# Kernel optimization log

Measured on AMD Instinct MI355X. Metric: run time of the kernel, lower is better.

Reference implementation:

```python
import jax, jax.numpy as jnp
import numpy as np

B, S, D, H = 4, 2048, 1024, 16
DK = D // H


def setup_inputs() -> dict:
    key = jax.random.key(0)
    ks = jax.random.split(key, 12)
    std = 0.02
    inp = {
        "query": jax.random.normal(ks[0], (B, S, D), jnp.float32),
        "key": jax.random.normal(ks[1], (B, S, D), jnp.float32),
        "value": jax.random.normal(ks[2], (B, S, D), jnp.float32),
        "mask": jnp.ones((B, 1, 1, S), jnp.int32),
        "Wq": jax.random.normal(ks[3], (D, D), jnp.float32) * std,
        "bq": jnp.zeros((D,), jnp.float32),
        "Wk": jax.random.normal(ks[4], (D, D), jnp.float32) * std,
        "bk": jnp.zeros((D,), jnp.float32),
        "Wv": jax.random.normal(ks[5], (D, D), jnp.float32) * std,
        "bv": jnp.zeros((D,), jnp.float32),
        "Wo": jax.random.normal(ks[6], (D, D), jnp.float32) * std,
        "bo": jnp.zeros((D,), jnp.float32),
    }
    return inp


def reference(query, key, value, mask, Wq, bq, Wk, bk, Wv, bv, Wo, bo):
    # nn.Linear: x @ W.T + b; then split heads -> [B, H, S, DK]
    def proj(x, W, b):
        y = x @ W.T + b
        return y.reshape(B, S, H, DK).transpose(0, 2, 1, 3)

    q = proj(query, Wq, bq)
    k = proj(key, Wk, bk)
    v = proj(value, Wv, bv)

    scale = 1.0 / jnp.sqrt(jnp.asarray(DK, q.dtype))
    scores = jnp.einsum('bhqd,bhkd->bhqk', q, k) * scale  # [B,H,S,S]
    scores = jnp.where(mask == 0, jnp.asarray(-1e9, scores.dtype), scores)
    p_attn = jax.nn.softmax(scores, axis=-1)  # dropout p=0 -> identity
    ctx = jnp.einsum('bhqk,bhkd->bhqd', p_attn, v)
    ctx = ctx.transpose(0, 2, 1, 3).reshape(B, S, D)
    out = ctx @ Wo.T + bo
    return out
```

## Files before the change

kernel.cpp:

```cpp
#include <hip/hip_runtime.h>

#define BB 4
#define SS 2048
#define DD 1024
#define HH 16
#define DKC 64
#define MT (BB*SS)

typedef _Float16 f16x8 __attribute__((ext_vector_type(8)));
typedef _Float16 f16x4 __attribute__((ext_vector_type(4)));
typedef float f32x4 __attribute__((ext_vector_type(4)));
typedef int   i32x4 __attribute__((ext_vector_type(4)));

__global__ __launch_bounds__(256) void cvt3(const float* __restrict__ s0,
                                            const float* __restrict__ s1,
                                            const float* __restrict__ s2,
                                            _Float16* __restrict__ dst, int n) {
  const float* src = (blockIdx.y == 0) ? s0 : ((blockIdx.y == 1) ? s1 : s2);
  _Float16* d = dst + (size_t)blockIdx.y * n;
  int i = (blockIdx.x * 256 + threadIdx.x) * 4;
  if (i < n) {
    f32x4 f = *(const f32x4*)(src + i);
    f16x4 o;
#pragma unroll
    for (int j = 0; j < 4; ++j) o[j] = (_Float16)f[j];
    *(f16x4*)(d + i) = o;
  }
}

__global__ __launch_bounds__(256) void cvt4(const float* __restrict__ s0,
                                            const float* __restrict__ s1,
                                            const float* __restrict__ s2,
                                            const float* __restrict__ s3,
                                            _Float16* __restrict__ dst, int n) {
  const float* src = (blockIdx.y == 0) ? s0 : ((blockIdx.y == 1) ? s1 :
                     ((blockIdx.y == 2) ? s2 : s3));
  _Float16* d = dst + (size_t)blockIdx.y * n;
  int i = (blockIdx.x * 256 + threadIdx.x) * 4;
  if (i < n) {
    f32x4 f = *(const f32x4*)(src + i);
    f16x4 o;
#pragma unroll
    for (int j = 0; j < 4; ++j) o[j] = (_Float16)f[j];
    *(f16x4*)(d + i) = o;
  }
}

__global__ __launch_bounds__(256) void gemm_qkv(const _Float16* __restrict__ Xb,
                                                const _Float16* __restrict__ Wb,
                                                const float* __restrict__ b0,
                                                const float* __restrict__ b1,
                                                const float* __restrict__ b2,
                                                _Float16* __restrict__ Pj) {
  const int z = blockIdx.z;
  const _Float16* A = Xb + (size_t)z * MT * DD;
  const _Float16* W = Wb + (size_t)z * DD * DD;
  const float* bias = (z == 0) ? b0 : ((z == 1) ? b1 : b2);
  _Float16* out = Pj + (size_t)z * MT * DD;

  const int m0 = blockIdx.x * 128;
  const int n0 = blockIdx.y * 128;
  const int t = threadIdx.x;
  const int lane = t & 63;
  const int wave = t >> 6;
  const int q = lane >> 4, r = lane & 15;
  const int wm = (wave & 1) * 64, wn = (wave >> 1) * 64;

  __shared__ __align__(16) _Float16 sA[128 * 32];
  __shared__ __align__(16) _Float16 sB[128 * 32];

  f32x4 acc[4][4] = {};

  const int row0 = t >> 2, cc = t & 3;

  f16x8 apre[2], bpre[2];
#pragma unroll
  for (int i = 0; i < 2; ++i) {
    int row = row0 + 64 * i;
    apre[i] = *(const f16x8*)(A + (size_t)(m0 + row) * DD + cc * 8);
    bpre[i] = *(const f16x8*)(W + (size_t)(n0 + row) * DD + cc * 8);
  }

  for (int k0 = 0; k0 < DD; k0 += 32) {
#pragma unroll
    for (int i = 0; i < 2; ++i) {
      int c = t + 256 * i;
      *(f16x8*)&sA[c * 8] = apre[i];
      *(f16x8*)&sB[c * 8] = bpre[i];
    }
    __syncthreads();

    if (k0 + 32 < DD) {
#pragma unroll
      for (int i = 0; i < 2; ++i) {
        int row = row0 + 64 * i;
        apre[i] = *(const f16x8*)(A + (size_t)(m0 + row) * DD + k0 + 32 + cc * 8);
        bpre[i] = *(const f16x8*)(W + (size_t)(n0 + row) * DD + k0 + 32 + cc * 8);
      }
    }

    f16x8 af[4], bf[4];
#pragma unroll
    for (int x = 0; x < 4; ++x) {
      af[x] = *(const f16x8*)&sA[(wm + x * 16 + r) * 32 + q * 8];
      bf[x] = *(const f16x8*)&sB[(wn + x * 16 + r) * 32 + q * 8];
    }
#pragma unroll
    for (int mi = 0; mi < 4; ++mi)
#pragma unroll
      for (int ni = 0; ni < 4; ++ni)
        acc[mi][ni] = __builtin_amdgcn_mfma_f32_16x16x32_f16(af[mi], bf[ni], acc[mi][ni], 0, 0, 0);
    __syncthreads();
  }

  if (z == 2) {
#pragma unroll
    for (int ni = 0; ni < 4; ++ni) {
      int gn = n0 + wn + ni * 16 + r;
      float bv = bias[gn];
      int h = gn >> 6, dk = gn & 63;
#pragma unroll
      for (int mi = 0; mi < 4; ++mi) {
        int gm = m0 + wm + mi * 16 + q * 4;
        int bb = gm >> 11, s = gm & 2047;
        f16x4 o4;
#pragma unroll
        for (int rr = 0; rr < 4; ++rr) o4[rr] = (_Float16)(acc[mi][ni][rr] + bv);
        *(f16x4*)&out[((size_t)((bb * HH + h) * DKC + dk)) * SS + s] = o4;
      }
    }
  } else {
#pragma unroll
    for (int ni = 0; ni < 4; ++ni) {
      int gn = n0 + wn + ni * 16 + r;
      float bv = bias[gn];
      int h = gn >> 6, dk = gn & 63;
#pragma unroll
      for (int mi = 0; mi < 4; ++mi) {
#pragma unroll
        for (int rr = 0; rr < 4; ++rr) {
          int gm = m0 + wm + mi * 16 + q * 4 + rr;
          int bb = gm >> 11, s = gm & 2047;
          out[((size_t)((bb * HH + h) * SS + s)) * DKC + dk] = (_Float16)(acc[mi][ni][rr] + bv);
        }
      }
    }
  }
}

__global__ __launch_bounds__(256) void attn(const _Float16* __restrict__ Pj,
                                            const int* __restrict__ mask,
                                            _Float16* __restrict__ Cx) {
  const int qt = blockIdx.x, h = blockIdx.y, bb = blockIdx.z;
  const size_t hoff = ((size_t)(bb * HH + h) * SS) * DKC;
  const _Float16* Qh  = Pj + hoff;
  const _Float16* Kh  = Pj + (size_t)MT * DD + hoff;
  const _Float16* Vth = Pj + (size_t)2 * MT * DD + hoff;
  _Float16* Ch = Cx + hoff;
  const int* mrow = mask + bb * SS;

  const int t = threadIdx.x, lane = t & 63, wave = t >> 6;
  const int q = lane >> 4, r = lane & 15;
  const int qrow0 = qt * 128 + wave * 32;

  __shared__ __align__(16) _Float16 sK[64 * 64];
  __shared__ __align__(16) _Float16 sVt[64 * 64];
  __shared__ __align__(16) _Float16 sP[4][32 * 64];
  __shared__ __align__(16) float    sMB[SS];

  {
    int i0 = t * 8;
    i32x4 m0v = *(const i32x4*)(mrow + i0);
    i32x4 m1v = *(const i32x4*)(mrow + i0 + 4);
    f32x4 b0v, b1v;
#pragma unroll
    for (int j = 0; j < 4; ++j) {
      b0v[j] = m0v[j] ? 0.0f : -1e30f;
      b1v[j] = m1v[j] ? 0.0f : -1e30f;
    }
    *(f32x4*)&sMB[i0] = b0v;
    *(f32x4*)&sMB[i0 + 4] = b1v;
  }

  f16x8 qf[2][2];
#pragma unroll
  for (int mi = 0; mi < 2; ++mi)
#pragma unroll
    for (int kk = 0; kk < 2; ++kk)
      qf[mi][kk] = *(const f16x8*)&Qh[(size_t)(qrow0 + mi * 16 + r) * DKC + kk * 32 + q * 8];

  float lst[2][4] = {};
  f32x4 oacc[2][4] = {};

  const float C2 = 0.125f * 1.44269504089f;

  const int srow0 = t >> 3, scc = t & 7;

  f16x8 kpre[2], vpre[2];
#pragma unroll
  for (int i = 0; i < 2; ++i) {
    int row = srow0 + 32 * i;
    kpre[i] = *(const f16x8*)(Kh + (size_t)row * DKC + scc * 8);
    vpre[i] = *(const f16x8*)(Vth + (size_t)row * SS + scc * 8);
  }

  for (int kt = 0; kt < SS; kt += 64) {
#pragma unroll
    for (int i = 0; i < 2; ++i) {
      int row = srow0 + 32 * i;
      int off = row * 64 + (((scc ^ (row & 7)) << 3));
      *(f16x8*)&sK [off] = kpre[i];
      *(f16x8*)&sVt[off] = vpre[i];
    }
    __syncthreads();

    if (kt + 64 < SS) {
#pragma unroll
      for (int i = 0; i < 2; ++i) {
        int row = srow0 + 32 * i;
        kpre[i] = *(const f16x8*)(Kh + (size_t)(kt + 64 + row) * DKC + scc * 8);
        vpre[i] = *(const f16x8*)(Vth + (size_t)row * SS + kt + 64 + scc * 8);
      }
    }

    f32x4 sacc[2][4] = {};
#pragma unroll
    for (int kk = 0; kk < 2; ++kk) {
      f16x8 kb[4];
#pragma unroll
      for (int ni = 0; ni < 4; ++ni)
        kb[ni] = *(const f16x8*)&sK[(ni * 16 + r) * 64 + ((((kk * 4 + q) ^ (r & 7)) << 3))];
#pragma unroll
      for (int mi = 0; mi < 2; ++mi)
#pragma unroll
        for (int ni = 0; ni < 4; ++ni)
          sacc[mi][ni] = __builtin_amdgcn_mfma_f32_16x16x32_f16(qf[mi][kk], kb[ni], sacc[mi][ni], 0, 0, 0);
    }

    float mb[4];
#pragma unroll
    for (int ni = 0; ni < 4; ++ni) mb[ni] = sMB[kt + ni * 16 + r];

#pragma unroll
    for (int mi = 0; mi < 2; ++mi) {
#pragma unroll
      for (int rr = 0; rr < 4; ++rr) {
        int rowoff = (mi * 16 + q * 4 + rr) * 64;
        int ksw = ((q << 1) | (rr & 1)) << 3;
#pragma unroll
        for (int ni = 0; ni < 4; ++ni) {
          float p = __builtin_amdgcn_exp2f(__builtin_fmaf(sacc[mi][ni][rr], C2, mb[ni]));
          lst[mi][rr] += p;
          sP[wave][rowoff + ((ni * 16 + r) ^ ksw)] = (_Float16)p;
        }
      }
    }
    __threadfence_block();

#pragma unroll
    for (int kk = 0; kk < 2; ++kk) {
      f16x8 ap[2], vb[4];
#pragma unroll
      for (int mi = 0; mi < 2; ++mi) {
        int row = mi * 16 + r;
        int ksw = ((((r >> 2) & 3) << 1) | (r & 1)) << 3;
        ap[mi] = *(const f16x8*)&sP[wave][row * 64 + ((kk * 32 + q * 8) ^ ksw)];
      }
#pragma unroll
      for (int ni = 0; ni < 4; ++ni) {
        vb[ni] = *(const f16x8*)&sVt[(ni * 16 + r) * 64 + ((((kk * 4 + q) ^ (r & 7)) << 3))];
      }
#pragma unroll
      for (int mi = 0; mi < 2; ++mi)
#pragma unroll
        for (int ni = 0; ni < 4; ++ni)
          oacc[mi][ni] = __builtin_amdgcn_mfma_f32_16x16x32_f16(ap[mi], vb[ni], oacc[mi][ni], 0, 0, 0);
    }
    __syncthreads();
  }

#pragma unroll
  for (int mi = 0; mi < 2; ++mi)
#pragma unroll
    for (int rr = 0; rr < 4; ++rr) {
      float l = lst[mi][rr];
#pragma unroll
      for (int d = 1; d < 16; d <<= 1) l += __shfl_xor(l, d);
      lst[mi][rr] = 1.0f / l;
    }

#pragma unroll
  for (int mi = 0; mi < 2; ++mi)
#pragma unroll
    for (int ni = 0; ni < 4; ++ni)
#pragma unroll
      for (int rr = 0; rr < 4; ++rr) {
        int row = qrow0 + mi * 16 + q * 4 + rr;
        Ch[(size_t)row * DKC + ni * 16 + r] = (_Float16)(oacc[mi][ni][rr] * lst[mi][rr]);
      }
}

__global__ __launch_bounds__(256) void gemm_out(const _Float16* __restrict__ Cx,
                                                const _Float16* __restrict__ W,
                                                const float* __restrict__ bias,
                                                float* __restrict__ out) {
  const int m0 = blockIdx.x * 128;
  const int n0 = blockIdx.y * 128;
  const int t = threadIdx.x;
  const int lane = t & 63;
  const int wave = t >> 6;
  const int q = lane >> 4, r = lane & 15;
  const int wm = (wave & 1) * 64, wn = (wave >> 1) * 64;

  __shared__ __align__(16) _Float16 sA[128 * 32];
  __shared__ __align__(16) _Float16 sB[128 * 32];

  f32x4 acc[4][4] = {};

  const int row0 = t >> 2, cc = t & 3;
  size_t abase[2];
#pragma unroll
  for (int i = 0; i < 2; ++i) {
    int gm = m0 + row0 + 64 * i;
    int bb = gm >> 11, s = gm & 2047;
    abase[i] = ((size_t)(bb * HH) * SS + s) * DKC;
  }

  f16x8 apre[2], bpre[2];
#pragma unroll
  for (int i = 0; i < 2; ++i) {
    apre[i] = *(const f16x8*)(Cx + abase[i] + cc * 8);
    bpre[i] = *(const f16x8*)(W + (size_t)(n0 + row0 + 64 * i) * DD + cc * 8);
  }

  for (int k0 = 0; k0 < DD; k0 += 32) {
#pragma unroll
    for (int i = 0; i < 2; ++i) {
      int c = t + 256 * i;
      *(f16x8*)&sA[c * 8] = apre[i];
      *(f16x8*)&sB[c * 8] = bpre[i];
    }
    __syncthreads();

    if (k0 + 32 < DD) {
      int k1 = k0 + 32;
      int head = k1 >> 6, off = (k1 & 63) + cc * 8;
#pragma unroll
      for (int i = 0; i < 2; ++i) {
        apre[i] = *(const f16x8*)(Cx + abase[i] + (size_t)head * SS * DKC + off);
        bpre[i] = *(const f16x8*)(W + (size_t)(n0 + row0 + 64 * i) * DD + k1 + cc * 8);
      }
    }

    f16x8 af[4], bf[4];
#pragma unroll
    for (int x = 0; x < 4; ++x) {
      af[x] = *(const f16x8*)&sA[(wm + x * 16 + r) * 32 + q * 8];
      bf[x] = *(const f16x8*)&sB[(wn + x * 16 + r) * 32 + q * 8];
    }
#pragma unroll
    for (int mi = 0; mi < 4; ++mi)
#pragma unroll
      for (int ni = 0; ni < 4; ++ni)
        acc[mi][ni] = __builtin_amdgcn_mfma_f32_16x16x32_f16(af[mi], bf[ni], acc[mi][ni], 0, 0, 0);
    __syncthreads();
  }

#pragma unroll
  for (int ni = 0; ni < 4; ++ni) {
    int gn = n0 + wn + ni * 16 + r;
    float bv = bias[gn];
#pragma unroll
    for (int mi = 0; mi < 4; ++mi) {
#pragma unroll
      for (int rr = 0; rr < 4; ++rr) {
        int gm = m0 + wm + mi * 16 + q * 4 + rr;
        out[(size_t)gm * DD + gn] = acc[mi][ni][rr] + bv;
      }
    }
  }
}

extern "C" void kernel_launch(void* const* d_in, const int* in_sizes, int n_in,
                              void* d_out, int out_size, void* d_ws, size_t ws_size,
                              hipStream_t stream) {
  const float* query = (const float*)d_in[0];
  const float* key_  = (const float*)d_in[1];
  const float* value = (const float*)d_in[2];
  const int*   mask  = (const int*)d_in[3];
  const float* Wq = (const float*)d_in[4];
  const float* bq = (const float*)d_in[5];
  const float* Wk = (const float*)d_in[6];
  const float* bk = (const float*)d_in[7];
  const float* Wv = (const float*)d_in[8];
  const float* bv = (const float*)d_in[9];
  const float* Wo = (const float*)d_in[10];
  const float* bo = (const float*)d_in[11];
  float* out = (float*)d_out;

  const int nX = MT * DD;
  const int nW = DD * DD;

  _Float16* Xb = (_Float16*)d_ws;
  _Float16* Wb = Xb + (size_t)3 * nX;
  _Float16* Pj = Wb + (size_t)4 * nW;
  _Float16* Cx = Pj + (size_t)3 * nX;

  cvt3<<<dim3(nX / 1024, 3), 256, 0, stream>>>(query, key_, value, Xb, nX);
  cvt4<<<dim3(nW / 1024, 4), 256, 0, stream>>>(Wq, Wk, Wv, Wo, Wb, nW);

  gemm_qkv<<<dim3(MT / 128, DD / 128, 3), 256, 0, stream>>>(Xb, Wb, bq, bk, bv, Pj);
  attn<<<dim3(SS / 128, HH, BB), 256, 0, stream>>>(Pj, mask, Cx);
  gemm_out<<<dim3(MT / 128, DD / 128), 256, 0, stream>>>(Cx, Wb + (size_t)3 * nW, bo, out);
}
```

Baseline: 382.0 us.

## Permute V^T key order to match P layout and pack P stores; merge convert kernels

Merges the two fp32-to-fp16 conversion kernels into one launch covering inputs and weights. The V-projection epilogue now writes V^T with a permuted key order within each 64-key block, so that the attention kernel can pack four probabilities with cvt_pkrtz and write them to shared memory as one 8-byte store instead of four scalar stores. The LDS swizzles for sVt and sP are simplified to match. The cost is scattered scalar global stores in the V epilogue and a switch to round-toward-zero conversion for P.

```diff
diff --git a/kernel.cpp b/kernel.cpp
--- a/kernel.cpp
+++ b/kernel.cpp
@@ -6,44 +6,40 @@
 #define HH 16
 #define DKC 64
 #define MT (BB*SS)
+#define NX (MT*DD)
+#define NW (DD*DD)
 
 typedef _Float16 f16x8 __attribute__((ext_vector_type(8)));
 typedef _Float16 f16x4 __attribute__((ext_vector_type(4)));
+typedef _Float16 f16x2 __attribute__((ext_vector_type(2)));
 typedef float f32x4 __attribute__((ext_vector_type(4)));
 typedef int   i32x4 __attribute__((ext_vector_type(4)));
 
-__global__ __launch_bounds__(256) void cvt3(const float* __restrict__ s0,
-                                            const float* __restrict__ s1,
-                                            const float* __restrict__ s2,
-                                            _Float16* __restrict__ dst, int n) {
-  const float* src = (blockIdx.y == 0) ? s0 : ((blockIdx.y == 1) ? s1 : s2);
-  _Float16* d = dst + (size_t)blockIdx.y * n;
-  int i = (blockIdx.x * 256 + threadIdx.x) * 4;
-  if (i < n) {
-    f32x4 f = *(const f32x4*)(src + i);
-    f16x4 o;
-#pragma unroll
-    for (int j = 0; j < 4; ++j) o[j] = (_Float16)f[j];
-    *(f16x4*)(d + i) = o;
-  }
-}
-
-__global__ __launch_bounds__(256) void cvt4(const float* __restrict__ s0,
-                                            const float* __restrict__ s1,
-                                            const float* __restrict__ s2,
-                                            const float* __restrict__ s3,
-                                            _Float16* __restrict__ dst, int n) {
-  const float* src = (blockIdx.y == 0) ? s0 : ((blockIdx.y == 1) ? s1 :
-                     ((blockIdx.y == 2) ? s2 : s3));
-  _Float16* d = dst + (size_t)blockIdx.y * n;
-  int i = (blockIdx.x * 256 + threadIdx.x) * 4;
-  if (i < n) {
-    f32x4 f = *(const f32x4*)(src + i);
-    f16x4 o;
-#pragma unroll
-    for (int j = 0; j < 4; ++j) o[j] = (_Float16)f[j];
-    *(f16x4*)(d + i) = o;
-  }
+__global__ __launch_bounds__(256) void cvt_all(const float* __restrict__ xq,
+                                               const float* __restrict__ xk,
+                                               const float* __restrict__ xv,
+                                               const float* __restrict__ wq,
+                                               const float* __restrict__ wk,
+                                               const float* __restrict__ wv,
+                                               const float* __restrict__ wo,
+                                               _Float16* __restrict__ dst) {
+  size_t i = ((size_t)blockIdx.x * 256 + threadIdx.x) * 4;
+  const float* src; size_t off;
+  if (i < (size_t)NX)          { src = xq; off = i; }
+  else if (i < (size_t)2*NX)   { src = xk; off = i - (size_t)NX; }
+  else if (i < (size_t)3*NX)   { src = xv; off = i - (size_t)2*NX; }
+  else {
+    size_t j = i - (size_t)3*NX;
+    if (j < (size_t)NW)        { src = wq; off = j; }
+    else if (j < (size_t)2*NW) { src = wk; off = j - (size_t)NW; }
+    else if (j < (size_t)3*NW) { src = wv; off = j - (size_t)2*NW; }
+    else                       { src = wo; off = j - (size_t)3*NW; }
+  }
+  f32x4 f = *(const f32x4*)(src + off);
+  f16x4 o;
+#pragma unroll
+  for (int j = 0; j < 4; ++j) o[j] = (_Float16)f[j];
+  *(f16x4*)(dst + i) = o;
 }
 
 __global__ __launch_bounds__(256) void gemm_qkv(const _Float16* __restrict__ Xb,
@@ -122,11 +118,13 @@
 #pragma unroll
       for (int mi = 0; mi < 4; ++mi) {
         int gm = m0 + wm + mi * 16 + q * 4;
-        int bb = gm >> 11, s = gm & 2047;
-        f16x4 o4;
-#pragma unroll
-        for (int rr = 0; rr < 4; ++rr) o4[rr] = (_Float16)(acc[mi][ni][rr] + bv);
-        *(f16x4*)&out[((size_t)((bb * HH + h) * DKC + dk)) * SS + s] = o4;
+        int bb = gm >> 11, s0 = gm & 2047;
+        int kl = s0 & 63;
+        int kap0 = (kl & 15) * 4 + (kl >> 4);
+        size_t base = ((size_t)((bb * HH + h) * DKC + dk)) * SS + (s0 - kl);
+#pragma unroll
+        for (int rr = 0; rr < 4; ++rr)
+          out[base + kap0 + rr * 4] = (_Float16)(acc[mi][ni][rr] + bv);
       }
     }
   } else {
@@ -208,9 +206,8 @@
 #pragma unroll
     for (int i = 0; i < 2; ++i) {
       int row = srow0 + 32 * i;
-      int off = row * 64 + (((scc ^ (row & 7)) << 3));
-      *(f16x8*)&sK [off] = kpre[i];
-      *(f16x8*)&sVt[off] = vpre[i];
+      *(f16x8*)&sK [row * 64 + ((scc ^ (row & 7)) << 3)]        = kpre[i];
+      *(f16x8*)&sVt[row * 64 + ((scc ^ ((row & 1) << 2)) << 3)] = vpre[i];
     }
     __syncthreads();
 
@@ -245,14 +242,17 @@
     for (int mi = 0; mi < 2; ++mi) {
 #pragma unroll
       for (int rr = 0; rr < 4; ++rr) {
-        int rowoff = (mi * 16 + q * 4 + rr) * 64;
-        int ksw = ((q << 1) | (rr & 1)) << 3;
-#pragma unroll
-        for (int ni = 0; ni < 4; ++ni) {
-          float p = __builtin_amdgcn_exp2f(__builtin_fmaf(sacc[mi][ni][rr], C2, mb[ni]));
-          lst[mi][rr] += p;
-          sP[wave][rowoff + ((ni * 16 + r) ^ ksw)] = (_Float16)p;
-        }
+        float pp[4];
+#pragma unroll
+        for (int ni = 0; ni < 4; ++ni)
+          pp[ni] = __builtin_amdgcn_exp2f(__builtin_fmaf(sacc[mi][ni][rr], C2, mb[ni]));
+        lst[mi][rr] += (pp[0] + pp[1]) + (pp[2] + pp[3]);
+        int prow = mi * 16 + q * 4 + rr;
+        int goff = prow * 64 + (((r >> 1) ^ ((rr & 1) << 2)) << 3) + ((r & 1) << 2);
+        unsigned lo = __builtin_bit_cast(unsigned, __builtin_amdgcn_cvt_pkrtz(pp[0], pp[1]));
+        unsigned hi = __builtin_bit_cast(unsigned, __builtin_amdgcn_cvt_pkrtz(pp[2], pp[3]));
+        uint2 u; u.x = lo; u.y = hi;
+        *(uint2*)&sP[wave][goff] = u;
       }
     }
     __threadfence_block();
@@ -263,12 +263,14 @@
 #pragma unroll
       for (int mi = 0; mi < 2; ++mi) {
         int row = mi * 16 + r;
-        int ksw = ((((r >> 2) & 3) << 1) | (r & 1)) << 3;
-        ap[mi] = *(const f16x8*)&sP[wave][row * 64 + ((kk * 32 + q * 8) ^ ksw)];
+        int g = ((kk * 4 + q) ^ ((r & 1) << 2)) << 3;
+        ap[mi] = *(const f16x8*)&sP[wave][row * 64 + g];
       }
 #pragma unroll
       for (int ni = 0; ni < 4; ++ni) {
-        vb[ni] = *(const f16x8*)&sVt[(ni * 16 + r) * 64 + ((((kk * 4 + q) ^ (r & 7)) << 3))];
+        int row = ni * 16 + r;
+        int g = ((kk * 4 + q) ^ ((r & 1) << 2)) << 3;
+        vb[ni] = *(const f16x8*)&sVt[row * 64 + g];
       }
 #pragma unroll
       for (int mi = 0; mi < 2; ++mi)
@@ -398,18 +400,14 @@
   const float* bo = (const float*)d_in[11];
   float* out = (float*)d_out;
 
-  const int nX = MT * DD;
-  const int nW = DD * DD;
-
   _Float16* Xb = (_Float16*)d_ws;
-  _Float16* Wb = Xb + (size_t)3 * nX;
-  _Float16* Pj = Wb + (size_t)4 * nW;
-  _Float16* Cx = Pj + (size_t)3 * nX;
-
-  cvt3<<<dim3(nX / 1024, 3), 256, 0, stream>>>(query, key_, value, Xb, nX);
-  cvt4<<<dim3(nW / 1024, 4), 256, 0, stream>>>(Wq, Wk, Wv, Wo, Wb, nW);
+  _Float16* Wb = Xb + (size_t)3 * NX;
+  _Float16* Pj = Wb + (size_t)4 * NW;
+  _Float16* Cx = Pj + (size_t)3 * NX;
+
+  cvt_all<<<(3 * NX + 4 * NW) / 1024, 256, 0, stream>>>(query, key_, value, Wq, Wk, Wv, Wo, Xb);
 
   gemm_qkv<<<dim3(MT / 128, DD / 128, 3), 256, 0, stream>>>(Xb, Wb, bq, bk, bv, Pj);
   attn<<<dim3(SS / 128, HH, BB), 256, 0, stream>>>(Pj, mask, Cx);
-  gemm_out<<<dim3(MT / 128, DD / 128), 256, 0, stream>>>(Cx, Wb + (size_t)3 * nW, bo, out);
+  gemm_out<<<dim3(MT / 128, DD / 128), 256, 0, stream>>>(Cx, Wb + (size_t)3 * NW, bo, out);
 }
```

Measured after the change: 380.0 us. About the same (-0.5%).
